# Kernel optimization log

Hardware: AMD Instinct MI355X
Metric: run time of the kernel (lower is better)

The kernel has to match this reference:

```python
import jax, jax.numpy as jnp
import numpy as np

N = 32            # batch (age.shape[0])
N_SAMPLE = 8
S = N * N_SAMPLE  # posterior samples
T = 1024          # len_param
K = 64            # len_window
D = 4             # dim_target
P = 8             # dim_param
LOG2PI = float(np.log(2.0 * np.pi))


def _windows(x, axis, num, size):
    # torch.unfold equivalent, but window axis inserted right after `axis`
    idx = jnp.arange(num)[:, None] + jnp.arange(size)[None, :]
    return jnp.take(x, idx, axis=axis)


def _coeffs(a_pad):
    # a_pad: (2K-2, D, 1) -> AR weight matrix d: (K, K, D)
    # d[t, k] = prod(a[t-K+1+k+1 .. t]) with trailing 1 (reversed cumprod of windows)
    b = _windows(a_pad, 0, K, K - 1)                              # (K, K-1, D, 1)
    c = jnp.flip(jnp.cumprod(jnp.flip(b, 1), axis=1), 1)
    d = jnp.concatenate([c, jnp.ones_like(c[:, :1])], axis=1)      # (K, K, D, 1)
    return d[..., 0]                                               # (K, K, D)


def _window_param(z, d):
    # z: (S, K, D, P); d: (K, K, D) -> param: (S, K, D, P)
    z_pad = jnp.pad(z, ((0, 0), (K - 1, 0), (0, 0), (0, 0)))
    zwin = _windows(z_pad, 1, K, K)                                # (S, K, K, D, P)
    return jnp.einsum('stkdp,tkd->stdp', zwin, d)


def _forward(m, s_raw, a_raw, noise, dim_idx):
    mm = m[:, dim_idx]                         # (T, D, P)
    s = jax.nn.softplus(s_raw[:, dim_idx])     # scale_transform
    a = jax.nn.sigmoid(a_raw[:, dim_idx])      # (T-1, D, 1)
    # ---- first window ----
    a_pad = jnp.pad(a[:K - 1], ((K - 1, 0), (0, 0), (0, 0)))       # (2K-2, D, 1)
    mean = (1.0 - a_pad[K - 2:]) * mm[:K]                          # (K, D, P)
    sw = s[:K]
    z = mean + sw * noise[:, :K]                                   # rsample
    lp = -jnp.log(sw) - 0.5 * LOG2PI - 0.5 * ((z - mean) / sw) ** 2
    param = _window_param(z, _coeffs(a_pad))
    params, lps = [param], [lp]
    # ---- subsequent windows (sequential carry via param[:, -1]) ----
    for l in range(K, T, K):
        r = min(l + K, T)
        aw = a[l - 1:r - 1]                                        # (K, D, 1)
        mean = (1.0 - aw) * mm[l:r]
        sw = s[l:r]
        z = mean + sw * noise[:, l:r]
        lp = -jnp.log(sw) - 0.5 * LOG2PI - 0.5 * ((z - mean) / sw) ** 2
        a_pad = jnp.pad(aw[1:], ((K - 1, 0), (0, 0), (0, 0)))
        p = _window_param(z, _coeffs(a_pad))
        p = p + jnp.cumprod(aw, axis=0)[None] * param[:, -1][:, None]
        params.append(p)
        lps.append(lp)
        param = p
    return jnp.concatenate(params, axis=1), jnp.concatenate(lps, axis=1)


def setup_inputs() -> dict:
    key = jax.random.key(0)
    k = jax.random.split(key, 6)
    return {
        'y': jax.random.normal(k[0], (1, T, D), dtype=jnp.float32),
        'age': jax.random.uniform(k[1], (N,), dtype=jnp.float32),
        'm': 0.1 * jax.random.normal(k[2], (T, D, P), dtype=jnp.float32),
        's_raw': 0.1 * jax.random.normal(k[3], (T, D, P), dtype=jnp.float32) - 6.0,
        'a_raw': jax.random.normal(k[4], (T - 1, D, 1), dtype=jnp.float32),
        'noise': jax.random.normal(k[5], (S, T, D, P), dtype=jnp.float32),
        'cond_sample': jnp.zeros((S, D, P), dtype=jnp.float32),
        'dim_idx': jnp.arange(D, dtype=jnp.int32),
        'compute_log_prob': 1,
    }


def reference(y, age, m, s_raw, a_raw, noise, cond_sample, dim_idx, compute_log_prob):
    param, log_prob = _forward(m, s_raw, a_raw, noise, dim_idx)
    if compute_log_prob:
        return (param, log_prob)
    return param
```

## Files before the change

### kernel.cpp

```cpp
#include <hip/hip_runtime.h>

#define T_DIM 1024
#define D_DIM 4
#define P_DIM 8
#define S_DIM 256
#define DP 32
#define TDP (T_DIM * DP)
#define LOG2PI_F 1.8378770664093453f

typedef float vf4 __attribute__((ext_vector_type(4)));

__device__ __forceinline__ float sigmoid_fast(float x) {
    return __builtin_amdgcn_rcpf(1.0f + __expf(-x));
}

__global__ __launch_bounds__(1024) void fused_scan(
    const float* __restrict__ noise,
    const float* __restrict__ m,
    const float* __restrict__ s_raw,
    const float* __restrict__ a_raw,
    const int* __restrict__ dim_idx,
    float* __restrict__ param_out,
    float* __restrict__ lp_out)
{
    const int tid  = threadIdx.x;
    const int qc   = tid & 7;
    const int cj   = tid >> 3;
    const int cjw  = cj & 7;
    const int wg   = tid >> 6;
    const int lane = tid & 63;

    const int d  = qc >> 1;
    const int p0 = (qc & 1) * 4;
    const int di = dim_idx[d];

    extern __shared__ __align__(16) float nls[];
    __shared__ float wtp[16][32];
    __shared__ float wtm8[16][8];
    __shared__ float wci[16][32];

    const size_t sbase = (size_t)blockIdx.x * TDP;
    const int    off0  = cj * 8 * DP + qc * 4;

    float* lbase = nls + wg * 2048;

#pragma unroll
    for (int k = 0; k < 8; ++k) {
        const float* g = noise + sbase + off0 + (size_t)k * DP;
        __builtin_amdgcn_global_load_lds(
            (const __attribute__((address_space(1))) void*)g,
            (__attribute__((address_space(3))) void*)(lbase + k * 256),
            16, 0, 0);
    }
    asm volatile("s_waitcnt vmcnt(0)" ::: "memory");

    float Mk[8];
    vf4   rp = (vf4){0.f, 0.f, 0.f, 0.f};
    float rm = 1.0f;
#pragma unroll
    for (int k = 0; k < 8; ++k) {
        const int t = cj * 8 + k;
        const int o = off0 + k * DP;
        const vf4 n  = *(const vf4*)(lbase + k * 256 + lane * 4);
        const vf4 mv = *(const vf4*)(m     + (t * D_DIM + di) * P_DIM + p0);
        const vf4 sr = *(const vf4*)(s_raw + (t * D_DIM + di) * P_DIM + p0);

        float A = 0.0f;
        if (t > 0) A = sigmoid_fast(a_raw[(t - 1) * D_DIM + di]);
        const float oma = 1.0f - A;

        vf4 sv, nl;
        sv.x = __logf(1.0f + __expf(sr.x));  nl.x = -__logf(sv.x) - 0.5f * LOG2PI_F;
        sv.y = __logf(1.0f + __expf(sr.y));  nl.y = -__logf(sv.y) - 0.5f * LOG2PI_F;
        sv.z = __logf(1.0f + __expf(sr.z));  nl.z = -__logf(sv.z) - 0.5f * LOG2PI_F;
        sv.w = __logf(1.0f + __expf(sr.w));  nl.w = -__logf(sv.w) - 0.5f * LOG2PI_F;

        vf4 lp;
        lp.x = nl.x - 0.5f * n.x * n.x;
        lp.y = nl.y - 0.5f * n.y * n.y;
        lp.z = nl.z - 0.5f * n.z * n.z;
        lp.w = nl.w - 0.5f * n.w * n.w;
        *(vf4*)(lp_out + sbase + o) = lp;

        vf4 z;
        z.x = oma * mv.x + sv.x * n.x;
        z.y = oma * mv.y + sv.y * n.y;
        z.z = oma * mv.z + sv.z * n.z;
        z.w = oma * mv.w + sv.w * n.w;

        rp.x = z.x + A * rp.x;
        rp.y = z.y + A * rp.y;
        rp.z = z.z + A * rp.z;
        rp.w = z.w + A * rp.w;
        rm  *= A;
        Mk[k] = rm;
        *(vf4*)(lbase + k * 256 + lane * 4) = rp;
    }

#pragma unroll
    for (int off = 1; off < 8; off <<= 1) {
        const int dd = off * 8;
        vf4 pp;
        pp.x = __shfl_up(rp.x, dd, 64);
        pp.y = __shfl_up(rp.y, dd, 64);
        pp.z = __shfl_up(rp.z, dd, 64);
        pp.w = __shfl_up(rp.w, dd, 64);
        const float pm = __shfl_up(rm, dd, 64);
        if (cjw >= off) {
            rp.x += rm * pp.x;
            rp.y += rm * pp.y;
            rp.z += rm * pp.z;
            rp.w += rm * pp.w;
            rm *= pm;
        }
    }

    if (cjw == 7) {
        *(vf4*)&wtp[wg][qc * 4] = rp;
        wtm8[wg][qc] = rm;
    }
    __syncthreads();
    if (tid < 32) {
        float c = 0.0f;
#pragma unroll
        for (int g = 0; g < 16; ++g) {
            wci[g][tid] = c;
            c = wtp[g][tid] + wtm8[g][tid >> 2] * c;
        }
    }
    __syncthreads();

    vf4 ep;
    ep.x = __shfl_up(rp.x, 8, 64);
    ep.y = __shfl_up(rp.y, 8, 64);
    ep.z = __shfl_up(rp.z, 8, 64);
    ep.w = __shfl_up(rp.w, 8, 64);
    float em = __shfl_up(rm, 8, 64);
    if (cjw == 0) {
        ep = (vf4){0.f, 0.f, 0.f, 0.f};
        em = 1.0f;
    }
    const vf4 ci = *(const vf4*)&wci[wg][qc * 4];
    vf4 carry;
    carry.x = ep.x + em * ci.x;
    carry.y = ep.y + em * ci.y;
    carry.z = ep.z + em * ci.z;
    carry.w = ep.w + em * ci.w;

#pragma unroll
    for (int k = 0; k < 8; ++k) {
        const int o = off0 + k * DP;
        const vf4 pl = *(const vf4*)(lbase + k * 256 + lane * 4);
        vf4 pv;
        pv.x = pl.x + Mk[k] * carry.x;
        pv.y = pl.y + Mk[k] * carry.y;
        pv.z = pl.z + Mk[k] * carry.z;
        pv.w = pl.w + Mk[k] * carry.w;
        *(vf4*)(param_out + sbase + o) = pv;
    }
}

extern "C" void kernel_launch(void* const* d_in, const int* in_sizes, int n_in,
                              void* d_out, int out_size, void* d_ws, size_t ws_size,
                              hipStream_t stream)
{
    const float* m      = (const float*)d_in[2];
    const float* s_raw  = (const float*)d_in[3];
    const float* a_raw  = (const float*)d_in[4];
    const float* noise  = (const float*)d_in[5];
    const int*   dimidx = (const int*)d_in[7];

    float* param_out = (float*)d_out;
    float* lp_out    = param_out + (size_t)S_DIM * TDP;

    fused_scan<<<S_DIM, 1024, 131072, stream>>>(noise, m, s_raw, a_raw, dimidx,
                                                param_out, lp_out);
}
```

Baseline: 116.5 us.

## Split each sample's time scan across two blocks with decoupled flag carry

Each sample is now handled by two 512-thread blocks, each covering half of the time axis, instead of one 1024-thread block. The second half waits on a global flag and reads the first half's carry totals from workspace through acquire/release atomics. The aim is more blocks and less LDS per block, which should raise occupancy and spread the 256 samples over more CUs. The cost is an extra memset launch and a spin-wait dependency between blocks. Correctness relies on the h=0 blocks being scheduled before or alongside the h=1 blocks, or the wait could deadlock.

```diff
diff --git a/kernel.cpp b/kernel.cpp
--- a/kernel.cpp
+++ b/kernel.cpp
@@ -6,6 +6,7 @@
 #define S_DIM 256
 #define DP 32
 #define TDP (T_DIM * DP)
+#define HALF_T 512
 #define LOG2PI_F 1.8378770664093453f
 
 typedef float vf4 __attribute__((ext_vector_type(4)));
@@ -14,14 +15,16 @@
     return __builtin_amdgcn_rcpf(1.0f + __expf(-x));
 }
 
-__global__ __launch_bounds__(1024) void fused_scan(
+__global__ __launch_bounds__(512) void fused_scan(
     const float* __restrict__ noise,
     const float* __restrict__ m,
     const float* __restrict__ s_raw,
     const float* __restrict__ a_raw,
     const int* __restrict__ dim_idx,
     float* __restrict__ param_out,
-    float* __restrict__ lp_out)
+    float* __restrict__ lp_out,
+    float* __restrict__ tot,
+    int* __restrict__ flags)
 {
     const int tid  = threadIdx.x;
     const int qc   = tid & 7;
@@ -30,17 +33,21 @@
     const int wg   = tid >> 6;
     const int lane = tid & 63;
 
+    const int s = blockIdx.x & 255;
+    const int h = blockIdx.x >> 8;
+
     const int d  = qc >> 1;
     const int p0 = (qc & 1) * 4;
     const int di = dim_idx[d];
 
     extern __shared__ __align__(16) float nls[];
-    __shared__ float wtp[16][32];
-    __shared__ float wtm8[16][8];
-    __shared__ float wci[16][32];
-
-    const size_t sbase = (size_t)blockIdx.x * TDP;
-    const int    off0  = cj * 8 * DP + qc * 4;
+    __shared__ float wtp[8][32];
+    __shared__ float wtm8[8][8];
+    __shared__ float wci[8][32];
+
+    const size_t sbase = (size_t)s * TDP;
+    const int    tbase = h * HALF_T + cj * 8;
+    const int    off0  = tbase * DP + qc * 4;
 
     float* lbase = nls + wg * 2048;
 
@@ -59,7 +66,7 @@
     float rm = 1.0f;
 #pragma unroll
     for (int k = 0; k < 8; ++k) {
-        const int t = cj * 8 + k;
+        const int t = tbase + k;
         const int o = off0 + k * DP;
         const vf4 n  = *(const vf4*)(lbase + k * 256 + lane * 4);
         const vf4 mv = *(const vf4*)(m     + (t * D_DIM + di) * P_DIM + p0);
@@ -121,11 +128,28 @@
     }
     __syncthreads();
     if (tid < 32) {
-        float c = 0.0f;
-#pragma unroll
-        for (int g = 0; g < 16; ++g) {
+        float c;
+        if (h == 0) {
+            c = 0.0f;
+        } else {
+            while (__hip_atomic_load(&flags[s], __ATOMIC_ACQUIRE,
+                                     __HIP_MEMORY_SCOPE_AGENT) == 0)
+                __builtin_amdgcn_s_sleep(8);
+            c = __hip_atomic_load(&tot[s * 32 + tid], __ATOMIC_RELAXED,
+                                  __HIP_MEMORY_SCOPE_AGENT);
+        }
+#pragma unroll
+        for (int g = 0; g < 8; ++g) {
             wci[g][tid] = c;
             c = wtp[g][tid] + wtm8[g][tid >> 2] * c;
+        }
+        if (h == 0) {
+            __hip_atomic_store(&tot[s * 32 + tid], c, __ATOMIC_RELAXED,
+                               __HIP_MEMORY_SCOPE_AGENT);
+            asm volatile("s_waitcnt vmcnt(0)" ::: "memory");
+            if (tid == 0)
+                __hip_atomic_store(&flags[s], 1, __ATOMIC_RELEASE,
+                                   __HIP_MEMORY_SCOPE_AGENT);
         }
     }
     __syncthreads();
@@ -173,6 +197,10 @@
     float* param_out = (float*)d_out;
     float* lp_out    = param_out + (size_t)S_DIM * TDP;
 
-    fused_scan<<<S_DIM, 1024, 131072, stream>>>(noise, m, s_raw, a_raw, dimidx,
-                                                param_out, lp_out);
+    float* tot   = (float*)d_ws;
+    int*   flags = (int*)(tot + S_DIM * 32);
+    hipMemsetAsync(flags, 0, S_DIM * sizeof(int), stream);
+
+    fused_scan<<<S_DIM * 2, 512, 65536, stream>>>(noise, m, s_raw, a_raw, dimidx,
+                                                  param_out, lp_out, tot, flags);
 }
```

Result: slower. 126.4 us (+8.6%).
